# Kernel tuning notes

Hardware: AMD Instinct MI355X
Metric: run time of the kernel (lower is better)

The kernel has to match this reference:

```python
import jax, jax.numpy as jnp
import numpy as np

N = 192            # image grid size (NxN)
N_SHOTS = 192
N_SAMPLES = 192
TWO_PI = 2.0 * np.pi
PIPE_ITERS = 3     # gpunufft default is ~10; 3 suffices for a CPU-runnable reference


def initialize_2D_radial(n_shots, n_samples):
    """Radial trajectory, k in [-0.5, 0.5), shape (n_shots*n_samples, 2)."""
    angles = np.pi * np.arange(n_shots) / n_shots
    radii = np.linspace(-0.5, 0.5, n_samples, endpoint=False)
    kx = radii[None, :] * np.cos(angles[:, None])
    ky = radii[None, :] * np.sin(angles[:, None])
    return np.stack([kx, ky], axis=-1).reshape(-1, 2).astype(np.float32)


def setup_inputs() -> dict:
    key = jax.random.key(0)
    x = jax.random.normal(key, (2, N, N), dtype=jnp.float32)  # real/imag image
    trajectory = jnp.asarray(initialize_2D_radial(N_SHOTS, N_SAMPLES))  # (M,2)
    return {"x": x, "trajectory": trajectory}


def _mats(traj):
    # Separable NDFT factors: exp(-2pi i k_x * px), exp(-2pi i k_y * py).
    # A: (M, N), B: (M, N); M*N complex64 ~= 57 MB each.
    p = jnp.arange(N, dtype=jnp.float32) - N / 2.0  # centered pixel coords
    A = jnp.exp(-1j * TWO_PI * traj[:, 0:1] * p[None, :])
    B = jnp.exp(-1j * TWO_PI * traj[:, 1:2] * p[None, :])
    return A.astype(jnp.complex64), B.astype(jnp.complex64)


def _op(img, A, B):
    # type-2 NUFFT (exact NDFT): image (N,N) -> kspace (M,)
    t = jnp.einsum('my,xy->mx', B, img)      # contract y first
    return jnp.einsum('mx,mx->m', A, t)


def _adj(d, A, B):
    # type-1 NUFFT adjoint: samples (M,) -> image (N,N)
    return jnp.einsum('mx,my->xy', jnp.conj(A) * d[:, None], jnp.conj(B))


def _pipe_density(A, B):
    # Pipe & Menon iterative density compensation: w <- w / |F F^H w|
    w = jnp.ones(A.shape[0], dtype=jnp.complex64)
    def body(i, w):
        q = _op(_adj(w, A, B), A, B)
        return w / jnp.maximum(jnp.abs(q), 1e-20)
    w = jax.lax.fori_loop(0, PIPE_ITERS, body, w)
    return jnp.abs(w)  # real positive weights


def reference(x, trajectory):
    img = (x[0] + 1j * x[1]).astype(jnp.complex64)  # (N,N) complex image
    A, B = _mats(trajectory)
    # density weights computed from detached trajectory (gpunufft init-time)
    traj_sg = jax.lax.stop_gradient(trajectory)
    Asg, Bsg = _mats(traj_sg)
    w = jax.lax.stop_gradient(_pipe_density(Asg, Bsg))
    kspace = _op(img, A, B)                       # forward NUFFT
    adjoint = _adj(w * kspace, A, B)              # density-compensated adjoint
    return jnp.stack([adjoint.real, adjoint.imag])  # (2,N,N) float32
```

## Files before the change

kernel.cpp:

```cpp
#include <hip/hip_runtime.h>
#include <math.h>


#define MTOT 36864
#define NPIX 192
#define SPLITS 128
#define GRP 64
#define NCH 36
#define PG 64

typedef __attribute__((ext_vector_type(8))) short s16x8;
typedef __attribute__((ext_vector_type(4))) float f32x4;
typedef __attribute__((ext_vector_type(4))) unsigned u32x4;

__device__ __forceinline__ f32x4 mfma_bf16(u32x4 a, u32x4 b, f32x4 c) {
    return __builtin_amdgcn_mfma_f32_16x16x32_bf16(
        __builtin_bit_cast(s16x8, a), __builtin_bit_cast(s16x8, b), c, 0, 0, 0);
}

__device__ __forceinline__ void g2l16(const void* g, void* l) {
    __builtin_amdgcn_global_load_lds(
        (const __attribute__((address_space(1))) void*)g,
        (__attribute__((address_space(3))) void*)l, 16, 0, 0);
}

__device__ __forceinline__ void split_pk(float a, float b, unsigned &hi, unsigned &lo) {
    const unsigned ua = __float_as_uint(a), ub = __float_as_uint(b);
    const unsigned ha = (ua + 0x8000u) & 0xffff0000u;
    const unsigned hb = (ub + 0x8000u) & 0xffff0000u;
    hi = (ha >> 16) | hb;
    const float la = a - __uint_as_float(ha);
    const float lb = b - __uint_as_float(hb);
    lo = ((__float_as_uint(la) + 0x8000u) >> 16) |
         ((__float_as_uint(lb) + 0x8000u) & 0xffff0000u);
}

__device__ __forceinline__ void ksplit(float k, float &kh, float &kl) {
    kh = __uint_as_float(__float_as_uint(k) & 0xfffff000u);
    kl = k - kh;
}
__device__ __forceinline__ float redphase(float kh, float kl, float p) {
    float r = kh * p;
    r -= rintf(r);
    r = fmaf(kl, p, r);
    return r;
}
__device__ __forceinline__ unsigned rot16(unsigned v) {
    return __builtin_amdgcn_alignbit(v, v, 16);
}
__device__ __forceinline__ int swz(int c) {
    return ((c ^ (c >> 2)) & 3) << 2;
}

__global__ void precompP_k(const float* __restrict__ traj, const int comp,
                           unsigned* __restrict__ PS) {
    const int m = blockIdx.x * 256 + threadIdx.x;
    const int c = blockIdx.y;
    float kh, kl; ksplit(traj[2 * m + comp], kh, kl);
    const float ph = redphase(kh, kl, (float)(c - 96));
    const float co = __builtin_amdgcn_cosf(ph);
    const float si = __builtin_amdgcn_sinf(ph);
    unsigned h, l; split_pk(co, -si, h, l);
    const int mc = m >> 4, mi = (m & 15) ^ swz(c);
    PS[(size_t)mc * 6144 + c * 16 + mi]        = h;
    PS[(size_t)mc * 6144 + 3072 + c * 16 + mi] = l;
}

__global__ void winit_k(float* __restrict__ wr, float* __restrict__ wi) {
    const int m = blockIdx.x * 256 + threadIdx.x;
    wr[m] = 1.f; wi[m] = 0.f;
}

__global__ __launch_bounds__(256) void adj_gemm_k(
    const float* __restrict__ traj,
    const float* __restrict__ dr_g, const float* __restrict__ di_g,
    const unsigned* __restrict__ BS, float* __restrict__ outP)
{
    __shared__ unsigned sE[2][2048];
    __shared__ unsigned sB[3][2048];
    __shared__ float kxA[576], drA[576], diA[576];
    const int tid = threadIdx.x;
    const int lane = tid & 63, wid = tid >> 6;
    const int l15 = lane & 15, qd = lane >> 4;
    const int L = blockIdx.x;
    const int xcd = L & 7, j = L >> 3;
    const int g = xcd * (GRP / 8) + j / 9;
    const int tile = j % 9;
    const int bx = tile % 3, by = tile / 3;
    const int wi = wid & 1, wj = wid >> 1;
    const int x0 = bx * 64 + wi * 32, y0 = by * 64 + wj * 32;
    float* outRe = outP + (size_t)g * (2 * MTOT);
    float* outIm = outRe + MTOT;

    #pragma unroll
    for (int rep = 0; rep < 3; ++rep) {
        const int idx = tid + rep * 256;
        if (idx < 576) {
            const int mg = (idx < 288) ? g * 288 + idx
                                       : (g + 64) * 288 + (idx - 288);
            kxA[idx] = traj[2 * mg];
            drA[idx] = dr_g[mg];
            diA[idx] = di_g[mg];
        }
    }

    f32x4 accRe[2][2], accIm[2][2];
    #pragma unroll
    for (int i = 0; i < 2; ++i)
        #pragma unroll
        for (int j2 = 0; j2 < 2; ++j2) {
            accRe[i][j2] = (f32x4){0.f, 0.f, 0.f, 0.f};
            accIm[i][j2] = (f32x4){0.f, 0.f, 0.f, 0.f};
        }

    const int cE_ = tid >> 2;
    const float pf = (float)(bx * 64 + cE_ - 96);
    const int miq = tid & 3;
    const int ewaddr = cE_ * 16 + ((miq ^ ((cE_ ^ (cE_ >> 2)) & 3)) << 2);

    #define ECOMP(c, eb)                                                   \
    {                                                                      \
        const int db = (c) * 16 + miq * 4;                                 \
        const f32x4 kx4 = *(const f32x4*)(kxA + db);                       \
        const f32x4 dr4 = *(const f32x4*)(drA + db);                       \
        const f32x4 di4 = *(const f32x4*)(diA + db);                       \
        u32x4 hv, lv;                                                      \
        _Pragma("unroll")                                                  \
        for (int jj = 0; jj < 4; ++jj) {                                   \
            float kh_, kl_; ksplit(kx4[jj], kh_, kl_);                     \
            const float ph_ = redphase(kh_, kl_, pf);                      \
            const float co_ = __builtin_amdgcn_cosf(ph_);                  \
            const float si_ = __builtin_amdgcn_sinf(ph_);                  \
            const float Er_ = co_ * dr4[jj] - si_ * di4[jj];               \
            const float Ei_ = co_ * di4[jj] + si_ * dr4[jj];               \
            unsigned h_, l_; split_pk(Er_, Ei_, h_, l_);                   \
            hv[jj] = h_; lv[jj] = l_;                                      \
        }                                                                  \
        *(u32x4*)(&sE[eb][ewaddr])        = hv;                            \
        *(u32x4*)(&sE[eb][1024 + ewaddr]) = lv;                            \
    }

    const size_t g18 = (size_t)g * 18;
    const int byo = by * 1024 + tid * 4;
    #define STAGEB(c, buf)                                                 \
    {                                                                      \
        const size_t id_ = (g18 + (c) + (((c) >= 18) ? 1134 : 0)) * 6144; \
        const unsigned* B0_ = BS + id_;                                    \
        g2l16(B0_ + byo,        &sB[buf][tid * 4]);                        \
        g2l16(B0_ + 3072 + byo, &sB[buf][1024 + tid * 4]);                 \
    }

    int eoff[2], boff[2];
    #pragma unroll
    for (int t = 0; t < 2; ++t) {
        const int cE = wi * 32 + t * 16 + l15;
        eoff[t] = cE * 16 + ((qd ^ ((cE ^ (cE >> 2)) & 3)) << 2);
        const int cB = wj * 32 + t * 16 + l15;
        boff[t] = cB * 16 + ((qd ^ ((cB ^ (cB >> 2)) & 3)) << 2);
    }

    STAGEB(0, 0);
    STAGEB(1, 1);
    __syncthreads();
    ECOMP(0, 0);

    for (int ch = 0; ch < NCH; ++ch) {
        if (ch + 2 < NCH) {
            const int rb3 = ch % 3;
            const int wb = (rb3 + 2 >= 3) ? rb3 - 1 : rb3 + 2;
            STAGEB(ch + 2, wb);
            asm volatile("s_waitcnt vmcnt(4)" ::: "memory");
        } else if (ch + 1 < NCH) {
            asm volatile("s_waitcnt vmcnt(2)" ::: "memory");
        } else {
            asm volatile("s_waitcnt vmcnt(0)" ::: "memory");
        }
        asm volatile("s_waitcnt lgkmcnt(0)" ::: "memory");
        __builtin_amdgcn_s_barrier();

        const unsigned* se = &sE[ch & 1][0];
        const unsigned* sb = &sB[ch % 3][0];
        u32x4 Eh[2], El[2], PhA[2], PlA[2];
        #pragma unroll
        for (int t = 0; t < 2; ++t) {
            Eh[t]  = *(const u32x4*)(se + eoff[t]);
            El[t]  = *(const u32x4*)(se + 1024 + eoff[t]);
            PhA[t] = *(const u32x4*)(sb + boff[t]);
            PlA[t] = *(const u32x4*)(sb + 1024 + boff[t]);
        }
        asm volatile("s_waitcnt lgkmcnt(0)" ::: "memory");
        __builtin_amdgcn_sched_barrier(0);
        __builtin_amdgcn_s_barrier();

        if (ch + 1 < NCH) ECOMP(ch + 1, (ch + 1) & 1);

        #pragma unroll
        for (int sj = 0; sj < 2; ++sj) {
            const u32x4 Ph = PhA[sj], Pl = PlA[sj];
            u32x4 Qh, Ql;
            #pragma unroll
            for (int r = 0; r < 4; ++r) {
                Qh[r] = rot16(Ph[r]) ^ 0x00008000u;
                Ql[r] = rot16(Pl[r]) ^ 0x00008000u;
            }
            #pragma unroll
            for (int si = 0; si < 2; ++si) {
                accRe[si][sj] = mfma_bf16(Eh[si], Ph, accRe[si][sj]);
                accRe[si][sj] = mfma_bf16(Eh[si], Pl, accRe[si][sj]);
                accRe[si][sj] = mfma_bf16(El[si], Ph, accRe[si][sj]);
                accIm[si][sj] = mfma_bf16(Eh[si], Qh, accIm[si][sj]);
                accIm[si][sj] = mfma_bf16(Eh[si], Ql, accIm[si][sj]);
                accIm[si][sj] = mfma_bf16(El[si], Qh, accIm[si][sj]);
            }
        }
    }
    #undef ECOMP
    #undef STAGEB

    #pragma unroll
    for (int si = 0; si < 2; ++si)
        #pragma unroll
        for (int sj = 0; sj < 2; ++sj)
            #pragma unroll
            for (int rg = 0; rg < 4; ++rg) {
                const int x = x0 + si * 16 + qd * 4 + rg;
                const int y = y0 + sj * 16 + l15;
                outRe[x * NPIX + y] = accRe[si][sj][rg];
                outIm[x * NPIX + y] = accIm[si][sj][rg];
            }
}

__device__ __forceinline__ void fw_stage_load(const unsigned* __restrict__ Ghi,
                                              const unsigned* __restrict__ Glo,
                                              int tid, int koff, u32x4 st[3]) {
    #pragma unroll
    for (int j = 0; j < 3; ++j) {
        const int li = tid + j * 576;
        if (li < 1536) {
            const int row = li >> 3, pl = (li >> 2) & 1, qt = li & 3;
            const unsigned* src = pl ? Glo : Ghi;
            st[j] = *(const u32x4*)(src + row * 192 + koff + qt * 4);
        }
    }
}
__device__ __forceinline__ void fw_stage_write(unsigned* sb, int tid, const u32x4 st[3]) {
    #pragma unroll
    for (int j = 0; j < 3; ++j) {
        const int li = tid + j * 576;
        if (li < 1536) {
            const int row = li >> 3, pl = (li >> 2) & 1, qt = li & 3;
            *(u32x4*)(sb + pl * 3840 + row * 20 + qt * 4) = st[j];
        }
    }
}

__global__ __launch_bounds__(576) void fwdq_k(
    const float* __restrict__ traj,
    const unsigned* __restrict__ Ghi, const unsigned* __restrict__ Glo,
    float* __restrict__ wre, float* __restrict__ wim,
    const int mode,
    float* __restrict__ qre, float* __restrict__ qim)
{
    __shared__ unsigned sG[2][2 * 3840];
    const int tid = threadIdx.x;
    const int lane = tid & 63, wid = tid >> 6;
    const int l15 = lane & 15, q = lane >> 4;
    const int m = (blockIdx.x * 9 + wid) * 16 + l15;
    const float2 kk = *(const float2*)(traj + 2 * m);
    float kxh, kxl, kyh, kyl;
    ksplit(kk.x, kxh, kxl);
    ksplit(kk.y, kyh, kyl);

    f32x4 tre[12], tim[12];
    #pragma unroll
    for (int i = 0; i < 12; ++i) {
        tre[i] = (f32x4){0.f, 0.f, 0.f, 0.f};
        tim[i] = (f32x4){0.f, 0.f, 0.f, 0.f};
    }

    float bc, bs;
    { const float ph = redphase(kyh, kyl, (float)(q * 4 - 96)); 
      bc = __builtin_amdgcn_cosf(ph); bs = __builtin_amdgcn_sinf(ph); }
    const float r1c = __builtin_amdgcn_cosf(kk.y), r1s = __builtin_amdgcn_sinf(kk.y);
    float r16c, r16s;
    { float g = kk.y * 16.f; g -= rintf(g);
      r16c = __builtin_amdgcn_cosf(g); r16s = __builtin_amdgcn_sinf(g); }

    u32x4 st[3];
    fw_stage_load(Ghi, Glo, tid, 0, st);
    fw_stage_write(&sG[0][0], tid, st);
    __syncthreads();

    for (int ch = 0; ch < 12; ++ch) {
        if (ch < 11) fw_stage_load(Ghi, Glo, tid, (ch + 1) * 16, st);

        u32x4 Ph, Pl, Qh, Ql;
        {
            float c = bc, s = bs;
            #pragma unroll
            for (int r = 0; r < 4; ++r) {
                unsigned h, l; split_pk(c, s, h, l);
                Ph[r] = h; Pl[r] = l;
                Qh[r] = rot16(h) ^ 0x00008000u;
                Ql[r] = rot16(l) ^ 0x00008000u;
                const float nc = c * r1c - s * r1s, ns = s * r1c + c * r1s;
                c = nc; s = ns;
            }
            const float nbc = bc * r16c - bs * r16s, nbs = bs * r16c + bc * r16s;
            bc = nbc; bs = nbs;
        }

        const unsigned* sb = &sG[ch & 1][0];
        #pragma unroll
        for (int si = 0; si < 12; ++si) {
            const int base = (si * 16 + l15) * 20 + q * 4;
            const u32x4 gh = *(const u32x4*)(sb + base);
            const u32x4 gl = *(const u32x4*)(sb + 3840 + base);
            tre[si] = mfma_bf16(gh, Ph, tre[si]);
            tre[si] = mfma_bf16(gh, Pl, tre[si]);
            tre[si] = mfma_bf16(gl, Ph, tre[si]);
            tim[si] = mfma_bf16(gh, Qh, tim[si]);
            tim[si] = mfma_bf16(gh, Ql, tim[si]);
            tim[si] = mfma_bf16(gl, Qh, tim[si]);
        }

        if (ch < 11) {
            fw_stage_write(&sG[(ch + 1) & 1][0], tid, st);
            __syncthreads();
        }
    }

    float qr = 0.f, qi = 0.f;
    {
        float g = kk.x * 16.f; g -= rintf(g);
        const float rc = __builtin_amdgcn_cosf(g), rs = __builtin_amdgcn_sinf(g);
        #pragma unroll
        for (int rg = 0; rg < 4; ++rg) {
            const float ph = redphase(kxh, kxl, (float)(q * 4 + rg - 96));
            float c = __builtin_amdgcn_cosf(ph), s = __builtin_amdgcn_sinf(ph);
            #pragma unroll
            for (int si = 0; si < 12; ++si) {
                const float tr = tre[si][rg], ti = tim[si][rg];
                qr += c * tr + s * ti;
                qi += c * ti - s * tr;
                const float nc = c * rc - s * rs, ns = s * rc + c * rs;
                c = nc; s = ns;
            }
        }
    }
    qr += __shfl_xor(qr, 16); qi += __shfl_xor(qi, 16);
    qr += __shfl_xor(qr, 32); qi += __shfl_xor(qi, 32);
    if (lane < 16) {
        if (mode == 0) {
            const float den = fmaxf(sqrtf(qr * qr + qi * qi), 1e-20f);
            wre[m] /= den; wim[m] /= den;
        } else {
            const float sc = sqrtf(wre[m] * wre[m] + wim[m] * wim[m]);
            qre[m] = qr * sc; qim[m] = qi * sc;
        }
    }
}

__global__ void presplit_k(const float* __restrict__ re, const float* __restrict__ im,
                           unsigned* __restrict__ Gh, unsigned* __restrict__ Gl) {
    const int e = blockIdx.x * 256 + threadIdx.x;
    unsigned h, l;
    split_pk(re[e], im[e], h, l);
    Gh[e] = h; Gl[e] = l;
}

__global__ void presplitP_k(const float* __restrict__ outP,
                            unsigned* __restrict__ Gh, unsigned* __restrict__ Gl) {
    const int e = blockIdx.x * 256 + threadIdx.x;
    float re = 0.f, im = 0.f;
    #pragma unroll 8
    for (int g = 0; g < PG; ++g) {
        re += outP[(size_t)g * (2 * MTOT) + e];
        im += outP[(size_t)g * (2 * MTOT) + MTOT + e];
    }
    unsigned h, l;
    split_pk(re, im, h, l);
    Gh[e] = h; Gl[e] = l;
}

__global__ void reduceOut_k(const float* __restrict__ outP, float* __restrict__ out) {
    const int e = blockIdx.x * 256 + threadIdx.x;
    float re = 0.f, im = 0.f;
    #pragma unroll 8
    for (int g = 0; g < PG; ++g) {
        re += outP[(size_t)g * (2 * MTOT) + e];
        im += outP[(size_t)g * (2 * MTOT) + MTOT + e];
    }
    out[e] = re; out[MTOT + e] = im;
}

extern "C" void kernel_launch(void* const* d_in, const int* in_sizes, int n_in,
                              void* d_out, int out_size, void* d_ws, size_t ws_size,
                              hipStream_t stream)
{
    const float* xin  = (const float*)d_in[0];
    const float* traj = (const float*)d_in[1];
    float* out = (float*)d_out;

    char* pb = (char*)d_ws;
    unsigned* BS = (unsigned*)pb; pb += (size_t)2304 * 6144 * 4;
    float* outP = (float*)pb; pb += (size_t)PG * 2 * MTOT * 4;
    float* wr   = (float*)pb; pb += MTOT * 4;
    float* wi   = (float*)pb; pb += MTOT * 4;
    float* dre  = (float*)pb; pb += MTOT * 4;
    float* dim_ = (float*)pb; pb += MTOT * 4;
    unsigned* Ghi = (unsigned*)pb; pb += MTOT * 4;
    unsigned* Glo = (unsigned*)pb; pb += MTOT * 4;

    precompP_k<<<dim3(MTOT / 256, NPIX), 256, 0, stream>>>(traj, 1, BS);
    winit_k<<<MTOT / 256, 256, 0, stream>>>(wr, wi);

    for (int it = 0; it < 3; ++it) {
        adj_gemm_k<<<9 * GRP, 256, 0, stream>>>(traj, wr, wi, BS, outP);
        presplitP_k<<<MTOT / 256, 256, 0, stream>>>(outP, Ghi, Glo);
        fwdq_k<<<256, 576, 0, stream>>>(traj, Ghi, Glo, wr, wi, 0, dre, dim_);
    }

    presplit_k<<<MTOT / 256, 256, 0, stream>>>(xin, xin + MTOT, Ghi, Glo);
    fwdq_k<<<256, 576, 0, stream>>>(traj, Ghi, Glo, wr, wi, 1, dre, dim_);
    adj_gemm_k<<<9 * GRP, 256, 0, stream>>>(traj, dre, dim_, BS, outP);
    reduceOut_k<<<MTOT / 256, 256, 0, stream>>>(outP, out);
}
```

Baseline: 461.3 us.

## Reuse precomputed B phase factors in forward kernel and reorder E computation

```diff
diff --git a/kernel.cpp b/kernel.cpp
--- a/kernel.cpp
+++ b/kernel.cpp
@@ -163,6 +163,7 @@
     STAGEB(1, 1);
     __syncthreads();
     ECOMP(0, 0);
+    asm volatile("s_waitcnt lgkmcnt(0)" ::: "memory");
 
     for (int ch = 0; ch < NCH; ++ch) {
         if (ch + 2 < NCH) {
@@ -175,8 +176,9 @@
         } else {
             asm volatile("s_waitcnt vmcnt(0)" ::: "memory");
         }
-        asm volatile("s_waitcnt lgkmcnt(0)" ::: "memory");
         __builtin_amdgcn_s_barrier();
+
+        if (ch + 1 < NCH) ECOMP(ch + 1, (ch + 1) & 1);
 
         const unsigned* se = &sE[ch & 1][0];
         const unsigned* sb = &sB[ch % 3][0];
@@ -191,8 +193,6 @@
         asm volatile("s_waitcnt lgkmcnt(0)" ::: "memory");
         __builtin_amdgcn_sched_barrier(0);
         __builtin_amdgcn_s_barrier();
-
-        if (ch + 1 < NCH) ECOMP(ch + 1, (ch + 1) & 1);
 
         #pragma unroll
         for (int sj = 0; sj < 2; ++sj) {
@@ -255,7 +255,7 @@
 }
 
 __global__ __launch_bounds__(576) void fwdq_k(
-    const float* __restrict__ traj,
+    const float* __restrict__ traj, const unsigned* __restrict__ BS,
     const unsigned* __restrict__ Ghi, const unsigned* __restrict__ Glo,
     float* __restrict__ wre, float* __restrict__ wim,
     const int mode,
@@ -265,11 +265,11 @@
     const int tid = threadIdx.x;
     const int lane = tid & 63, wid = tid >> 6;
     const int l15 = lane & 15, q = lane >> 4;
-    const int m = (blockIdx.x * 9 + wid) * 16 + l15;
-    const float2 kk = *(const float2*)(traj + 2 * m);
-    float kxh, kxl, kyh, kyl;
-    ksplit(kk.x, kxh, kxl);
-    ksplit(kk.y, kyh, kyl);
+    const int mc = blockIdx.x * 9 + wid;
+    const int m = mc * 16 + l15;
+    const float kx = traj[2 * m];
+    float kxh, kxl;
+    ksplit(kx, kxh, kxl);
 
     f32x4 tre[12], tim[12];
     #pragma unroll
@@ -278,13 +278,15 @@
         tim[i] = (f32x4){0.f, 0.f, 0.f, 0.f};
     }
 
-    float bc, bs;
-    { const float ph = redphase(kyh, kyl, (float)(q * 4 - 96)); 
-      bc = __builtin_amdgcn_cosf(ph); bs = __builtin_amdgcn_sinf(ph); }
-    const float r1c = __builtin_amdgcn_cosf(kk.y), r1s = __builtin_amdgcn_sinf(kk.y);
-    float r16c, r16s;
-    { float g = kk.y * 16.f; g -= rintf(g);
-      r16c = __builtin_amdgcn_cosf(g); r16s = __builtin_amdgcn_sinf(g); }
+    const unsigned* Bm = BS + (size_t)mc * 6144;
+    int od[4];
+    #pragma unroll
+    for (int r = 0; r < 4; ++r)
+        od[r] = (q * 4 + r) * 16 + (l15 ^ (((r ^ q) & 3) << 2));
+
+    unsigned Wh[4], Wl[4];
+    #pragma unroll
+    for (int r = 0; r < 4; ++r) { Wh[r] = Bm[od[r]]; Wl[r] = Bm[3072 + od[r]]; }
 
     u32x4 st[3];
     fw_stage_load(Ghi, Glo, tid, 0, st);
@@ -295,19 +297,18 @@
         if (ch < 11) fw_stage_load(Ghi, Glo, tid, (ch + 1) * 16, st);
 
         u32x4 Ph, Pl, Qh, Ql;
-        {
-            float c = bc, s = bs;
-            #pragma unroll
-            for (int r = 0; r < 4; ++r) {
-                unsigned h, l; split_pk(c, s, h, l);
-                Ph[r] = h; Pl[r] = l;
-                Qh[r] = rot16(h) ^ 0x00008000u;
-                Ql[r] = rot16(l) ^ 0x00008000u;
-                const float nc = c * r1c - s * r1s, ns = s * r1c + c * r1s;
-                c = nc; s = ns;
-            }
-            const float nbc = bc * r16c - bs * r16s, nbs = bs * r16c + bc * r16s;
-            bc = nbc; bs = nbs;
+        #pragma unroll
+        for (int r = 0; r < 4; ++r) {
+            Ph[r] = Wh[r] ^ 0x80000000u;
+            Pl[r] = Wl[r] ^ 0x80000000u;
+            Qh[r] = rot16(Wh[r]);
+            Ql[r] = rot16(Wl[r]);
+        }
+        unsigned Nh[4], Nl[4];
+        if (ch < 11) {
+            const unsigned* Bn = Bm + (ch + 1) * 256;
+            #pragma unroll
+            for (int r = 0; r < 4; ++r) { Nh[r] = Bn[od[r]]; Nl[r] = Bn[3072 + od[r]]; }
         }
 
         const unsigned* sb = &sG[ch & 1][0];
@@ -327,12 +328,14 @@
         if (ch < 11) {
             fw_stage_write(&sG[(ch + 1) & 1][0], tid, st);
             __syncthreads();
+            #pragma unroll
+            for (int r = 0; r < 4; ++r) { Wh[r] = Nh[r]; Wl[r] = Nl[r]; }
         }
     }
 
     float qr = 0.f, qi = 0.f;
     {
-        float g = kk.x * 16.f; g -= rintf(g);
+        float g = kx * 16.f; g -= rintf(g);
         const float rc = __builtin_amdgcn_cosf(g), rs = __builtin_amdgcn_sinf(g);
         #pragma unroll
         for (int rg = 0; rg < 4; ++rg) {
@@ -418,11 +421,11 @@
     for (int it = 0; it < 3; ++it) {
         adj_gemm_k<<<9 * GRP, 256, 0, stream>>>(traj, wr, wi, BS, outP);
         presplitP_k<<<MTOT / 256, 256, 0, stream>>>(outP, Ghi, Glo);
-        fwdq_k<<<256, 576, 0, stream>>>(traj, Ghi, Glo, wr, wi, 0, dre, dim_);
+        fwdq_k<<<256, 576, 0, stream>>>(traj, BS, Ghi, Glo, wr, wi, 0, dre, dim_);
     }
 
     presplit_k<<<MTOT / 256, 256, 0, stream>>>(xin, xin + MTOT, Ghi, Glo);
-    fwdq_k<<<256, 576, 0, stream>>>(traj, Ghi, Glo, wr, wi, 1, dre, dim_);
+    fwdq_k<<<256, 576, 0, stream>>>(traj, BS, Ghi, Glo, wr, wi, 1, dre, dim_);
     adj_gemm_k<<<9 * GRP, 256, 0, stream>>>(traj, dre, dim_, BS, outP);
     reduceOut_k<<<MTOT / 256, 256, 0, stream>>>(outP, out);
 }
```

After: 458.5 us. Within noise of the previous version (-0.6%).
